# Optimization experiments

Measured on AMD Instinct MI355X. Metric: run time of the kernel, lower is better.

Reference implementation:

```python
import jax, jax.numpy as jnp
import numpy as np

T = 3
R = 0.05  # threshold on SQUARED distance (as in the source: dis < r)
N, M = 4, 384

_PSPEC = [("hW1", (3, 64)), ("hb1", (64,)), ("hW2", (64, 128)), ("hb2", (128,)), ("hW3", (128, 3)), ("hb3", (3,)),
          ("fW1", (6, 64)), ("fb1", (64,)), ("fW2", (64, 128)), ("fb2", (128,)), ("fW3", (128, 128)), ("fb3", (128,)),
          ("gW1", (128, 64)), ("gb1", (64,)), ("gW2", (64, 32)), ("gb2", (32,)), ("gW3", (32, 3)), ("gb3", (3,))]


def setup_inputs() -> dict:
    key = jax.random.key(0)
    inp = {"x": jax.random.uniform(key, (N, M, 3), jnp.float32)}
    for i, (name, shp) in enumerate(_PSPEC):
        k = jax.random.fold_in(key, i + 1)
        scale = 1.0 / np.sqrt(shp[0]) if len(shp) == 2 else 0.01
        inp[name] = jax.random.normal(k, (T,) + shp, jnp.float32) * jnp.float32(scale)
    return inp


def _mlp(x, W1, b1, W2, b2, W3, b3, final_relu):
    h = jax.nn.relu(x @ W1 + b1)
    h = jax.nn.relu(h @ W2 + b2)
    o = h @ W3 + b3
    return jax.nn.relu(o) if final_relu else o


def _forward(x, hW1, hb1, hW2, hb2, hW3, hb3, fW1, fb1, fW2, fb2, fW3, fb3, gW1, gb1, gW2, gb2, gW3, gb3):
    n, m, _ = x.shape
    diff = x[:, :, None, :] - x[:, None, :, :]              # (N,M,M,3)
    adj = jnp.sum(diff * diff, axis=-1) < R                 # (N,M,M) squared-dist ball
    state = x
    for t in range(T):
        # NOTE on MLP_h / delta: in the source, xj and xi inside getTimeEdges are
        # IDENTICAL broadcasts of xi_delta (both x.unsqueeze(-2).repeat over dim -2),
        # so xi[adj] = xj[adj] - xi[adj] == 0 everywhere. The relative-position
        # slot is therefore exactly zeros and delta = MLP_h(state) never affects
        # the output (and receives zero gradient in torch as well).
        rel = jnp.zeros((n, m, m, 3), x.dtype)
        # state[n,i,j,:] = state[n,j,:] where adj[n,i,j], else 0
        sfull = jnp.where(adj[..., None], state[:, None, :, :], 0.0)  # (N,M,M,3)
        eij = jnp.concatenate([rel, sfull], axis=-1)                   # (N,M,M,6)
        e = _mlp(eij, fW1[t], fb1[t], fW2[t], fb2[t], fW3[t], fb3[t], True)  # (N,M,M,128)
        e = jnp.where(adj[..., None], e, 0.0)
        agg = jnp.max(e, axis=2)                                       # max over neighbors j -> (N,M,128)
        state = _mlp(agg, gW1[t], gb1[t], gW2[t], gb2[t], gW3[t], gb3[t], True) + state
    return state


def reference(x, hW1, hb1, hW2, hb2, hW3, hb3, fW1, fb1, fW2, fb2, fW3, fb3, gW1, gb1, gW2, gb2, gW3, gb3):
    return _forward(x, hW1, hb1, hW2, hb2, hW3, hb3, fW1, fb1, fW2, fb2, fW3, fb3, gW1, gb1, gW2, gb2, gW3, gb3)
```

## Files before the change

### kernel.cpp

```cpp
#include <hip/hip_runtime.h>

#define MNODES 384
#define RTHRESH 0.05f


__device__ __forceinline__ void phi_stage(
    const float* __restrict__ fW1, const float* __restrict__ fb1,
    const float* __restrict__ fW2, const float* __restrict__ fb2,
    const float* __restrict__ fW3, const float* __restrict__ fb3,
    float s0, float s1, float s2, int lane,
    float* __restrict__ H1, float* __restrict__ H2,
    float* __restrict__ phidst )
{
    float v = fb1[lane];
    v = fmaf(s0, fW1[3 * 64 + lane], v);
    v = fmaf(s1, fW1[4 * 64 + lane], v);
    v = fmaf(s2, fW1[5 * 64 + lane], v);
    H1[lane] = fmaxf(v, 0.0f);
    float a0 = fb2[lane], a1 = fb2[lane + 64];
#pragma unroll 16
    for (int c = 0; c < 64; ++c) {
        const float h = H1[c];
        a0 = fmaf(h, fW2[c * 128 + lane], a0);
        a1 = fmaf(h, fW2[c * 128 + lane + 64], a1);
    }
    H2[lane] = fmaxf(a0, 0.0f);
    H2[lane + 64] = fmaxf(a1, 0.0f);
    float c0 = fb3[lane], c1 = fb3[lane + 64];
#pragma unroll 16
    for (int c = 0; c < 128; ++c) {
        const float h = H2[c];
        c0 = fmaf(h, fW3[c * 128 + lane], c0);
        c1 = fmaf(h, fW3[c * 128 + lane + 64], c1);
    }
    phidst[lane] = fmaxf(c0, 0.0f);
    phidst[lane + 64] = fmaxf(c1, 0.0f);
}

__global__ __launch_bounds__(256) void adj_phi0_kernel(
    const float* __restrict__ x,
    const float* __restrict__ fW1, const float* __restrict__ fb1,
    const float* __restrict__ fW2, const float* __restrict__ fb2,
    const float* __restrict__ fW3, const float* __restrict__ fb3,
    int* __restrict__ cnt, unsigned short* __restrict__ lists,
    float* __restrict__ phiA)
{
    __shared__ float xs[MNODES * 3];
    __shared__ float work[4][192];
    const int tid = threadIdx.x;
    const int wv = tid >> 6, lane = tid & 63;
    const int node = blockIdx.x * 4 + wv;
    const int n = blockIdx.x / 96;
    const int i = node - n * MNODES;

    for (int idx = tid; idx < MNODES * 3; idx += 256)
        xs[idx] = x[n * MNODES * 3 + idx];
    __syncthreads();

    const float s0 = xs[i * 3], s1 = xs[i * 3 + 1], s2 = xs[i * 3 + 2];
    unsigned short* ml = lists + (size_t)node * MNODES;
    int nc = 0;
#pragma unroll
    for (int rep = 0; rep < 6; ++rep) {
        const int j = rep * 64 + lane;
        float dx = xs[j * 3] - s0;
        float dy = xs[j * 3 + 1] - s1;
        float dz = xs[j * 3 + 2] - s2;
        float d2 = __fadd_rn(__fadd_rn(__fmul_rn(dx, dx), __fmul_rn(dy, dy)),
                             __fmul_rn(dz, dz));
        const bool a = d2 < RTHRESH;
        const unsigned long long m = __ballot(a);
        if (a) ml[nc + __popcll(m & ((1ull << lane) - 1ull))] = (unsigned short)j;
        nc += (int)__popcll(m);
    }
    if (lane == 0) cnt[node] = nc;

    phi_stage(fW1, fb1, fW2, fb2, fW3, fb3, s0, s1, s2, lane,
              &work[wv][0], &work[wv][64], phiA + (size_t)node * 128);
}

__global__ __launch_bounds__(256) void step_kernel(
    const float* __restrict__ phisrc, float* __restrict__ phidst,
    const int* __restrict__ cnt, const unsigned short* __restrict__ lists,
    const float* __restrict__ statesrc, float* __restrict__ statedst,
    const float* __restrict__ gW1, const float* __restrict__ gb1,
    const float* __restrict__ gW2, const float* __restrict__ gb2,
    const float* __restrict__ gW3, const float* __restrict__ gb3,
    const float* __restrict__ fW1n, const float* __restrict__ fb1n,
    const float* __restrict__ fW2n, const float* __restrict__ fb2n,
    const float* __restrict__ fW3n, const float* __restrict__ fb3n,
    int do_phi)
{
    __shared__ float work[4][224];
    const int tid = threadIdx.x;
    const int wv = tid >> 6, lane = tid & 63;
    const int node = __builtin_amdgcn_readfirstlane(blockIdx.x * 4 + wv);
    const int nbase = (blockIdx.x / 96) * MNODES;
    const int nc = cnt[node];
    const unsigned short* ml = lists + (size_t)node * MNODES;
    const float* pb = phisrc + (size_t)nbase * 128;
    float* const aggL = &work[wv][0];
    float* const h1L  = &work[wv][128];
    float* const h2L  = &work[wv][192];

    float m[8], p[8];
#pragma unroll
    for (int k = 0; k < 8; ++k) { m[k] = 0.0f; p[k] = 0.0f; }
    const int last = nc - 1;
    for (int jj = 0; jj < nc; jj += 8) {
        const float* r[8];
#pragma unroll
        for (int k = 0; k < 8; ++k) {
            const int jc = jj + k;
            const int j = ml[jc < last ? jc : last];
            r[k] = pb + (size_t)j * 128;
        }
#pragma unroll
        for (int k = 0; k < 8; ++k) {
            m[k] = fmaxf(m[k], r[k][lane]);
            p[k] = fmaxf(p[k], r[k][lane + 64]);
        }
    }
    aggL[lane] = fmaxf(fmaxf(fmaxf(m[0], m[1]), fmaxf(m[2], m[3])),
                       fmaxf(fmaxf(m[4], m[5]), fmaxf(m[6], m[7])));
    aggL[lane + 64] = fmaxf(fmaxf(fmaxf(p[0], p[1]), fmaxf(p[2], p[3])),
                            fmaxf(fmaxf(p[4], p[5]), fmaxf(p[6], p[7])));

    float h = gb1[lane];
#pragma unroll 16
    for (int c = 0; c < 128; ++c) h = fmaf(aggL[c], gW1[c * 64 + lane], h);
    h1L[lane] = fmaxf(h, 0.0f);
    if (lane < 32) {
        float v2 = gb2[lane];
#pragma unroll 16
        for (int k = 0; k < 64; ++k) v2 = fmaf(h1L[k], gW2[k * 32 + lane], v2);
        h2L[lane] = fmaxf(v2, 0.0f);
    }
    float sv = 0.0f;
    if (lane < 3) sv = statesrc[node * 3 + lane];
    float ns = 0.0f;
    if (lane < 3) {
        float v3 = gb3[lane];
#pragma unroll
        for (int q = 0; q < 32; ++q) v3 = fmaf(h2L[q], gW3[q * 3 + lane], v3);
        ns = fmaxf(v3, 0.0f) + sv;
        statedst[node * 3 + lane] = ns;
    }
    if (do_phi) {
        const float s0 = __shfl(ns, 0), s1 = __shfl(ns, 1), s2 = __shfl(ns, 2);
        phi_stage(fW1n, fb1n, fW2n, fb2n, fW3n, fb3n, s0, s1, s2, lane,
                  &work[wv][0], &work[wv][64], phidst + (size_t)node * 128);
    }
}

extern "C" void kernel_launch(void* const* d_in, const int* in_sizes, int n_in,
                              void* d_out, int out_size, void* d_ws, size_t ws_size,
                              hipStream_t stream) {
    const float* x   = (const float*)d_in[0];
    const float* fW1 = (const float*)d_in[7];
    const float* fb1 = (const float*)d_in[8];
    const float* fW2 = (const float*)d_in[9];
    const float* fb2 = (const float*)d_in[10];
    const float* fW3 = (const float*)d_in[11];
    const float* fb3 = (const float*)d_in[12];
    const float* gW1 = (const float*)d_in[13];
    const float* gb1 = (const float*)d_in[14];
    const float* gW2 = (const float*)d_in[15];
    const float* gb2 = (const float*)d_in[16];
    const float* gW3 = (const float*)d_in[17];
    const float* gb3 = (const float*)d_in[18];

    char* ws = (char*)d_ws;
    unsigned short* lists = (unsigned short*)(ws + 0);
    int* cnt              = (int*)(ws + 1179648);
    float* phiA           = (float*)(ws + 1185792);
    float* phiB           = (float*)(ws + 1972224);
    float* stateA         = (float*)(ws + 2758656);
    float* stateB         = (float*)(ws + 2777088);
    float* outp           = (float*)d_out;

    adj_phi0_kernel<<<384, 256, 0, stream>>>(x, fW1, fb1, fW2, fb2, fW3, fb3,
                                             cnt, lists, phiA);
    step_kernel<<<384, 256, 0, stream>>>(phiA, phiB, cnt, lists, x, stateA,
                                         gW1, gb1, gW2, gb2, gW3, gb3,
                                         fW1 + 384, fb1 + 64, fW2 + 8192, fb2 + 128,
                                         fW3 + 16384, fb3 + 128, 1);
    step_kernel<<<384, 256, 0, stream>>>(phiB, phiA, cnt, lists, stateA, stateB,
                                         gW1 + 8192, gb1 + 64, gW2 + 2048, gb2 + 32,
                                         gW3 + 96, gb3 + 3,
                                         fW1 + 768, fb1 + 128, fW2 + 16384, fb2 + 256,
                                         fW3 + 32768, fb3 + 256, 1);
    step_kernel<<<384, 256, 0, stream>>>(phiA, phiB, cnt, lists, stateB, outp,
                                         gW1 + 16384, gb1 + 128, gW2 + 4096, gb2 + 64,
                                         gW3 + 192, gb3 + 6,
                                         fW1, fb1, fW2, fb2, fW3, fb3, 0);
}
```

Baseline: 133.8 us.

## Process two nodes per single-wave block to reuse MLP weight loads

```diff
diff --git a/kernel.cpp b/kernel.cpp
--- a/kernel.cpp
+++ b/kernel.cpp
@@ -4,40 +4,49 @@
 #define RTHRESH 0.05f
 
 
-__device__ __forceinline__ void phi_stage(
+__device__ __forceinline__ void phi2_stage(
     const float* __restrict__ fW1, const float* __restrict__ fb1,
     const float* __restrict__ fW2, const float* __restrict__ fb2,
     const float* __restrict__ fW3, const float* __restrict__ fb3,
-    float s0, float s1, float s2, int lane,
-    float* __restrict__ H1, float* __restrict__ H2,
-    float* __restrict__ phidst )
+    float sa0, float sa1, float sa2,
+    float sb0, float sb1, float sb2,
+    int lane,
+    float (*H1)[64], float (*H2)[128],
+    float* __restrict__ rowA, float* __restrict__ rowB)
 {
-    float v = fb1[lane];
-    v = fmaf(s0, fW1[3 * 64 + lane], v);
-    v = fmaf(s1, fW1[4 * 64 + lane], v);
-    v = fmaf(s2, fW1[5 * 64 + lane], v);
-    H1[lane] = fmaxf(v, 0.0f);
-    float a0 = fb2[lane], a1 = fb2[lane + 64];
+    const float w3 = fW1[3 * 64 + lane];
+    const float w4 = fW1[4 * 64 + lane];
+    const float w5 = fW1[5 * 64 + lane];
+    const float bb = fb1[lane];
+    float va = fmaf(sa2, w5, fmaf(sa1, w4, fmaf(sa0, w3, bb)));
+    float vb = fmaf(sb2, w5, fmaf(sb1, w4, fmaf(sb0, w3, bb)));
+    H1[0][lane] = fmaxf(va, 0.0f);
+    H1[1][lane] = fmaxf(vb, 0.0f);
+    const float2 b2 = ((const float2*)fb2)[lane];
+    float a00 = b2.x, a01 = b2.y, a10 = b2.x, a11 = b2.y;
 #pragma unroll 16
     for (int c = 0; c < 64; ++c) {
-        const float h = H1[c];
-        a0 = fmaf(h, fW2[c * 128 + lane], a0);
-        a1 = fmaf(h, fW2[c * 128 + lane + 64], a1);
-    }
-    H2[lane] = fmaxf(a0, 0.0f);
-    H2[lane + 64] = fmaxf(a1, 0.0f);
-    float c0 = fb3[lane], c1 = fb3[lane + 64];
+        const float2 w = ((const float2*)(fW2 + c * 128))[lane];
+        const float h0 = H1[0][c], h1 = H1[1][c];
+        a00 = fmaf(h0, w.x, a00); a01 = fmaf(h0, w.y, a01);
+        a10 = fmaf(h1, w.x, a10); a11 = fmaf(h1, w.y, a11);
+    }
+    ((float2*)H2[0])[lane] = make_float2(fmaxf(a00, 0.0f), fmaxf(a01, 0.0f));
+    ((float2*)H2[1])[lane] = make_float2(fmaxf(a10, 0.0f), fmaxf(a11, 0.0f));
+    const float2 b3 = ((const float2*)fb3)[lane];
+    float c00 = b3.x, c01 = b3.y, c10 = b3.x, c11 = b3.y;
 #pragma unroll 16
     for (int c = 0; c < 128; ++c) {
-        const float h = H2[c];
-        c0 = fmaf(h, fW3[c * 128 + lane], c0);
-        c1 = fmaf(h, fW3[c * 128 + lane + 64], c1);
-    }
-    phidst[lane] = fmaxf(c0, 0.0f);
-    phidst[lane + 64] = fmaxf(c1, 0.0f);
-}
-
-__global__ __launch_bounds__(256) void adj_phi0_kernel(
+        const float2 w = ((const float2*)(fW3 + c * 128))[lane];
+        const float h0 = H2[0][c], h1 = H2[1][c];
+        c00 = fmaf(h0, w.x, c00); c01 = fmaf(h0, w.y, c01);
+        c10 = fmaf(h1, w.x, c10); c11 = fmaf(h1, w.y, c11);
+    }
+    ((float2*)rowA)[lane] = make_float2(fmaxf(c00, 0.0f), fmaxf(c01, 0.0f));
+    ((float2*)rowB)[lane] = make_float2(fmaxf(c10, 0.0f), fmaxf(c11, 0.0f));
+}
+
+__global__ __launch_bounds__(64) void adj_phi0_kernel(
     const float* __restrict__ x,
     const float* __restrict__ fW1, const float* __restrict__ fb1,
     const float* __restrict__ fW2, const float* __restrict__ fb2,
@@ -46,40 +55,54 @@
     float* __restrict__ phiA)
 {
     __shared__ float xs[MNODES * 3];
-    __shared__ float work[4][192];
-    const int tid = threadIdx.x;
-    const int wv = tid >> 6, lane = tid & 63;
-    const int node = blockIdx.x * 4 + wv;
-    const int n = blockIdx.x / 96;
-    const int i = node - n * MNODES;
-
-    for (int idx = tid; idx < MNODES * 3; idx += 256)
-        xs[idx] = x[n * MNODES * 3 + idx];
-    __syncthreads();
-
-    const float s0 = xs[i * 3], s1 = xs[i * 3 + 1], s2 = xs[i * 3 + 2];
-    unsigned short* ml = lists + (size_t)node * MNODES;
-    int nc = 0;
-#pragma unroll
-    for (int rep = 0; rep < 6; ++rep) {
-        const int j = rep * 64 + lane;
-        float dx = xs[j * 3] - s0;
-        float dy = xs[j * 3 + 1] - s1;
-        float dz = xs[j * 3 + 2] - s2;
-        float d2 = __fadd_rn(__fadd_rn(__fmul_rn(dx, dx), __fmul_rn(dy, dy)),
-                             __fmul_rn(dz, dz));
-        const bool a = d2 < RTHRESH;
-        const unsigned long long m = __ballot(a);
-        if (a) ml[nc + __popcll(m & ((1ull << lane) - 1ull))] = (unsigned short)j;
-        nc += (int)__popcll(m);
-    }
-    if (lane == 0) cnt[node] = nc;
-
-    phi_stage(fW1, fb1, fW2, fb2, fW3, fb3, s0, s1, s2, lane,
-              &work[wv][0], &work[wv][64], phiA + (size_t)node * 128);
-}
-
-__global__ __launch_bounds__(256) void step_kernel(
+    __shared__ float H1[2][64];
+    __shared__ float H2[2][128];
+    const int lane = threadIdx.x;
+    const int blk = blockIdx.x;
+    const int batch = blk & 3;
+    const int i0 = (blk >> 2) * 2;
+    const int g0 = batch * MNODES + i0;
+
+    {
+        const float4* src = (const float4*)(x + batch * MNODES * 3);
+        float4* dst = (float4*)xs;
+#pragma unroll
+        for (int k = 0; k < 5; ++k) {
+            const int idx = lane + k * 64;
+            if (idx < 288) dst[idx] = src[idx];
+        }
+    }
+
+    const float sa0 = xs[i0 * 3 + 0], sa1 = xs[i0 * 3 + 1], sa2 = xs[i0 * 3 + 2];
+    const float sb0 = xs[i0 * 3 + 3], sb1 = xs[i0 * 3 + 4], sb2 = xs[i0 * 3 + 5];
+
+#pragma unroll
+    for (int r = 0; r < 2; ++r) {
+        const float q0 = r ? sb0 : sa0, q1 = r ? sb1 : sa1, q2 = r ? sb2 : sa2;
+        unsigned short* ml = lists + (size_t)(g0 + r) * MNODES;
+        int nc = 0;
+#pragma unroll
+        for (int rep = 0; rep < 6; ++rep) {
+            const int j = rep * 64 + lane;
+            float dx = xs[j * 3 + 0] - q0;
+            float dy = xs[j * 3 + 1] - q1;
+            float dz = xs[j * 3 + 2] - q2;
+            float d2 = __fadd_rn(__fadd_rn(__fmul_rn(dx, dx), __fmul_rn(dy, dy)),
+                                 __fmul_rn(dz, dz));
+            const bool a = d2 < RTHRESH;
+            const unsigned long long m = __ballot(a);
+            if (a) ml[nc + __popcll(m & ((1ull << lane) - 1ull))] = (unsigned short)j;
+            nc += (int)__popcll(m);
+        }
+        if (lane == 0) cnt[g0 + r] = nc;
+    }
+
+    phi2_stage(fW1, fb1, fW2, fb2, fW3, fb3,
+               sa0, sa1, sa2, sb0, sb1, sb2, lane, H1, H2,
+               phiA + (size_t)g0 * 128, phiA + (size_t)(g0 + 1) * 128);
+}
+
+__global__ __launch_bounds__(64) void step_kernel(
     const float* __restrict__ phisrc, float* __restrict__ phidst,
     const int* __restrict__ cnt, const unsigned short* __restrict__ lists,
     const float* __restrict__ statesrc, float* __restrict__ statedst,
@@ -91,65 +114,96 @@
     const float* __restrict__ fW3n, const float* __restrict__ fb3n,
     int do_phi)
 {
-    __shared__ float work[4][224];
-    const int tid = threadIdx.x;
-    const int wv = tid >> 6, lane = tid & 63;
-    const int node = __builtin_amdgcn_readfirstlane(blockIdx.x * 4 + wv);
-    const int nbase = (blockIdx.x / 96) * MNODES;
-    const int nc = cnt[node];
-    const unsigned short* ml = lists + (size_t)node * MNODES;
-    const float* pb = phisrc + (size_t)nbase * 128;
-    float* const aggL = &work[wv][0];
-    float* const h1L  = &work[wv][128];
-    float* const h2L  = &work[wv][192];
-
-    float m[8], p[8];
-#pragma unroll
-    for (int k = 0; k < 8; ++k) { m[k] = 0.0f; p[k] = 0.0f; }
-    const int last = nc - 1;
-    for (int jj = 0; jj < nc; jj += 8) {
-        const float* r[8];
-#pragma unroll
-        for (int k = 0; k < 8; ++k) {
-            const int jc = jj + k;
-            const int j = ml[jc < last ? jc : last];
-            r[k] = pb + (size_t)j * 128;
-        }
-#pragma unroll
-        for (int k = 0; k < 8; ++k) {
-            m[k] = fmaxf(m[k], r[k][lane]);
-            p[k] = fmaxf(p[k], r[k][lane + 64]);
-        }
-    }
-    aggL[lane] = fmaxf(fmaxf(fmaxf(m[0], m[1]), fmaxf(m[2], m[3])),
-                       fmaxf(fmaxf(m[4], m[5]), fmaxf(m[6], m[7])));
-    aggL[lane + 64] = fmaxf(fmaxf(fmaxf(p[0], p[1]), fmaxf(p[2], p[3])),
-                            fmaxf(fmaxf(p[4], p[5]), fmaxf(p[6], p[7])));
-
-    float h = gb1[lane];
-#pragma unroll 16
-    for (int c = 0; c < 128; ++c) h = fmaf(aggL[c], gW1[c * 64 + lane], h);
-    h1L[lane] = fmaxf(h, 0.0f);
+    __shared__ float aggL[2][128];
+    __shared__ float h1L[2][64];
+    __shared__ float h2L[2][32];
+    __shared__ float H1[2][64];
+    __shared__ float H2[2][128];
+    const int lane = threadIdx.x;
+    const int blk = blockIdx.x;
+    const int batch = blk & 3;
+    const int g0 = batch * MNODES + (blk >> 2) * 2;
+
+    const int nc0 = cnt[g0], nc1 = cnt[g0 + 1];
+    const unsigned short* ml0 = lists + (size_t)g0 * MNODES;
+    const unsigned short* ml1 = ml0 + MNODES;
+    const float2* pb = (const float2*)(phisrc + (size_t)batch * MNODES * 128);
+
+    float mx0[8], my0[8], mx1[8], my1[8];
+#pragma unroll
+    for (int k = 0; k < 8; ++k) { mx0[k] = my0[k] = mx1[k] = my1[k] = 0.0f; }
+    {
+        const int last0 = nc0 - 1, last1 = nc1 - 1;
+        const int ncm = nc0 > nc1 ? nc0 : nc1;
+        for (int jj = 0; jj < ncm; jj += 8) {
+            const float2 *r0[8], *r1[8];
+#pragma unroll
+            for (int k = 0; k < 8; ++k) {
+                const int a = jj + k;
+                const int j0 = ml0[a < last0 ? a : last0];
+                const int j1 = ml1[a < last1 ? a : last1];
+                r0[k] = pb + (size_t)j0 * 64;
+                r1[k] = pb + (size_t)j1 * 64;
+            }
+#pragma unroll
+            for (int k = 0; k < 8; ++k) {
+                const float2 v0 = r0[k][lane], v1 = r1[k][lane];
+                mx0[k] = fmaxf(mx0[k], v0.x); my0[k] = fmaxf(my0[k], v0.y);
+                mx1[k] = fmaxf(mx1[k], v1.x); my1[k] = fmaxf(my1[k], v1.y);
+            }
+        }
+    }
+    ((float2*)aggL[0])[lane] = make_float2(
+        fmaxf(fmaxf(fmaxf(mx0[0], mx0[1]), fmaxf(mx0[2], mx0[3])),
+              fmaxf(fmaxf(mx0[4], mx0[5]), fmaxf(mx0[6], mx0[7]))),
+        fmaxf(fmaxf(fmaxf(my0[0], my0[1]), fmaxf(my0[2], my0[3])),
+              fmaxf(fmaxf(my0[4], my0[5]), fmaxf(my0[6], my0[7]))));
+    ((float2*)aggL[1])[lane] = make_float2(
+        fmaxf(fmaxf(fmaxf(mx1[0], mx1[1]), fmaxf(mx1[2], mx1[3])),
+              fmaxf(fmaxf(mx1[4], mx1[5]), fmaxf(mx1[6], mx1[7]))),
+        fmaxf(fmaxf(fmaxf(my1[0], my1[1]), fmaxf(my1[2], my1[3])),
+              fmaxf(fmaxf(my1[4], my1[5]), fmaxf(my1[6], my1[7]))));
+
+    float hA = gb1[lane], hB = hA;
+#pragma unroll 16
+    for (int c = 0; c < 128; ++c) {
+        const float w = gW1[c * 64 + lane];
+        hA = fmaf(aggL[0][c], w, hA);
+        hB = fmaf(aggL[1][c], w, hB);
+    }
+    h1L[0][lane] = fmaxf(hA, 0.0f);
+    h1L[1][lane] = fmaxf(hB, 0.0f);
     if (lane < 32) {
-        float v2 = gb2[lane];
-#pragma unroll 16
-        for (int k = 0; k < 64; ++k) v2 = fmaf(h1L[k], gW2[k * 32 + lane], v2);
-        h2L[lane] = fmaxf(v2, 0.0f);
-    }
-    float sv = 0.0f;
-    if (lane < 3) sv = statesrc[node * 3 + lane];
-    float ns = 0.0f;
+        float vA = gb2[lane], vB = vA;
+#pragma unroll 16
+        for (int k = 0; k < 64; ++k) {
+            const float w = gW2[k * 32 + lane];
+            vA = fmaf(h1L[0][k], w, vA);
+            vB = fmaf(h1L[1][k], w, vB);
+        }
+        h2L[0][lane] = fmaxf(vA, 0.0f);
+        h2L[1][lane] = fmaxf(vB, 0.0f);
+    }
+    float nsA = 0.0f, nsB = 0.0f;
     if (lane < 3) {
-        float v3 = gb3[lane];
-#pragma unroll
-        for (int q = 0; q < 32; ++q) v3 = fmaf(h2L[q], gW3[q * 3 + lane], v3);
-        ns = fmaxf(v3, 0.0f) + sv;
-        statedst[node * 3 + lane] = ns;
+        float oA = gb3[lane], oB = oA;
+#pragma unroll
+        for (int q = 0; q < 32; ++q) {
+            const float w = gW3[q * 3 + lane];
+            oA = fmaf(h2L[0][q], w, oA);
+            oB = fmaf(h2L[1][q], w, oB);
+        }
+        nsA = fmaxf(oA, 0.0f) + statesrc[g0 * 3 + lane];
+        nsB = fmaxf(oB, 0.0f) + statesrc[(g0 + 1) * 3 + lane];
+        statedst[g0 * 3 + lane] = nsA;
+        statedst[(g0 + 1) * 3 + lane] = nsB;
     }
     if (do_phi) {
-        const float s0 = __shfl(ns, 0), s1 = __shfl(ns, 1), s2 = __shfl(ns, 2);
-        phi_stage(fW1n, fb1n, fW2n, fb2n, fW3n, fb3n, s0, s1, s2, lane,
-                  &work[wv][0], &work[wv][64], phidst + (size_t)node * 128);
+        const float sa0 = __shfl(nsA, 0), sa1 = __shfl(nsA, 1), sa2 = __shfl(nsA, 2);
+        const float sb0 = __shfl(nsB, 0), sb1 = __shfl(nsB, 1), sb2 = __shfl(nsB, 2);
+        phi2_stage(fW1n, fb1n, fW2n, fb2n, fW3n, fb3n,
+                   sa0, sa1, sa2, sb0, sb1, sb2, lane, H1, H2,
+                   phidst + (size_t)g0 * 128, phidst + (size_t)(g0 + 1) * 128);
     }
 }
 
@@ -179,19 +233,19 @@
     float* stateB         = (float*)(ws + 2777088);
     float* outp           = (float*)d_out;
 
-    adj_phi0_kernel<<<384, 256, 0, stream>>>(x, fW1, fb1, fW2, fb2, fW3, fb3,
-                                             cnt, lists, phiA);
-    step_kernel<<<384, 256, 0, stream>>>(phiA, phiB, cnt, lists, x, stateA,
-                                         gW1, gb1, gW2, gb2, gW3, gb3,
-                                         fW1 + 384, fb1 + 64, fW2 + 8192, fb2 + 128,
-                                         fW3 + 16384, fb3 + 128, 1);
-    step_kernel<<<384, 256, 0, stream>>>(phiB, phiA, cnt, lists, stateA, stateB,
-                                         gW1 + 8192, gb1 + 64, gW2 + 2048, gb2 + 32,
-                                         gW3 + 96, gb3 + 3,
-                                         fW1 + 768, fb1 + 128, fW2 + 16384, fb2 + 256,
-                                         fW3 + 32768, fb3 + 256, 1);
-    step_kernel<<<384, 256, 0, stream>>>(phiA, phiB, cnt, lists, stateB, outp,
-                                         gW1 + 16384, gb1 + 128, gW2 + 4096, gb2 + 64,
-                                         gW3 + 192, gb3 + 6,
-                                         fW1, fb1, fW2, fb2, fW3, fb3, 0);
-}
+    adj_phi0_kernel<<<768, 64, 0, stream>>>(x, fW1, fb1, fW2, fb2, fW3, fb3,
+                                            cnt, lists, phiA);
+    step_kernel<<<768, 64, 0, stream>>>(phiA, phiB, cnt, lists, x, stateA,
+                                        gW1, gb1, gW2, gb2, gW3, gb3,
+                                        fW1 + 384, fb1 + 64, fW2 + 8192, fb2 + 128,
+                                        fW3 + 16384, fb3 + 128, 1);
+    step_kernel<<<768, 64, 0, stream>>>(phiB, phiA, cnt, lists, stateA, stateB,
+                                        gW1 + 8192, gb1 + 64, gW2 + 2048, gb2 + 32,
+                                        gW3 + 96, gb3 + 3,
+                                        fW1 + 768, fb1 + 128, fW2 + 16384, fb2 + 256,
+                                        fW3 + 32768, fb3 + 256, 1);
+    step_kernel<<<768, 64, 0, stream>>>(phiA, phiB, cnt, lists, stateB, outp,
+                                        gW1 + 16384, gb1 + 128, gW2 + 4096, gb2 + 64,
+                                        gW3 + 192, gb3 + 6,
+                                        fW1, fb1, fW2, fb2, fW3, fb3, 0);
+}
```

Result: no change. 134.9 us (+0.8%).
